# Kernel optimization log

Hardware: AMD Instinct MI355X
Metric: run time of the kernel (lower is better)

## Reference

```python
import jax, jax.numpy as jnp
import numpy as np

N = 50000      # num nodes
HID = 64       # hidden_dim
N2V = 64       # node2vec dim
E = 800000     # num edges
EP = 100000    # prediction edges
L = 2          # num_layers
EPS = 1e-5     # BatchNorm eps


def setup_inputs() -> dict:
    key = jax.random.key(0)
    ks = jax.random.split(key, 8)
    edge_index = jax.random.randint(ks[0], (2, E), 0, N)
    pred_edge = jax.random.randint(ks[1], (EP, 2), 0, N)
    id_emb = jax.random.normal(ks[2], (N, HID), jnp.float32) * 0.1      # learnable ID embedding
    n2v_emb = jax.random.normal(ks[3], (N, N2V), jnp.float32) * 0.1     # frozen node2vec embedding
    proj_w = jax.random.normal(ks[4], (HID + N2V, HID), jnp.float32) / np.sqrt(HID + N2V)
    proj_b = jnp.zeros((HID,), jnp.float32)
    conv_w = jax.random.normal(ks[5], (L, HID, HID), jnp.float32) / np.sqrt(HID)
    conv_b = jnp.zeros((L, HID), jnp.float32)
    bn_gamma = jnp.ones((L, HID), jnp.float32)
    bn_beta = jnp.zeros((L, HID), jnp.float32)
    return {"edge_index": edge_index, "pred_edge": pred_edge, "id_emb": id_emb,
            "n2v_emb": n2v_emb, "proj_w": proj_w, "proj_b": proj_b,
            "conv_w": conv_w, "conv_b": conv_b, "bn_gamma": bn_gamma, "bn_beta": bn_beta}


def reference(edge_index, pred_edge, id_emb, n2v_emb, proj_w, proj_b, conv_w, conv_b, bn_gamma, bn_beta):
    # input projection of concatenated embeddings: [N, HID+N2V] @ [HID+N2V, HID]
    x = jnp.concatenate([id_emb, n2v_emb], axis=1) @ proj_w + proj_b

    # GCN normalization with self-loops: norm_e = d^-1/2[src] * d^-1/2[dst]
    loops = jnp.arange(N, dtype=edge_index.dtype)
    row = jnp.concatenate([edge_index[0], loops])   # source nodes
    col = jnp.concatenate([edge_index[1], loops])   # destination nodes
    deg = jax.ops.segment_sum(jnp.ones(row.shape, x.dtype), col, num_segments=N)
    dis = jnp.where(deg > 0, jax.lax.rsqrt(deg), 0.0)
    norm = dis[row] * dis[col]                      # [E+N]

    for l in range(L):
        h = x @ conv_w[l]                                                    # [N, HID]
        agg = jax.ops.segment_sum(norm[:, None] * h[row], col, num_segments=N) + conv_b[l]
        # BatchNorm1d (training-mode batch stats over nodes)
        mu = agg.mean(axis=0)
        var = agg.var(axis=0)
        xn = (agg - mu) * jax.lax.rsqrt(var + EPS) * bn_gamma[l] + bn_beta[l]
        x = x + jax.nn.relu(xn)                                              # residual (shapes match)

    # dot-product link decoder
    z = x
    return (z[pred_edge[:, 0]] * z[pred_edge[:, 1]]).sum(axis=1)
```

## Files before the change

### kernel.cpp

```cpp
#include <hip/hip_runtime.h>

#define NN 50000
#define HID 64
#define NE 800000
#define NP 100000
#define BN_EPS 1e-5f
#define NB1 196

static inline size_t alignup(size_t x) { return (x + 255) & ~(size_t)255; }

__device__ __forceinline__ void f4fma(float a, const float4& w, float4& c) {
    c.x += a * w.x; c.y += a * w.y; c.z += a * w.z; c.w += a * w.w;
}
__device__ __forceinline__ void f4add(const float4& a, float4& c) {
    c.x += a.x; c.y += a.y; c.z += a.z; c.w += a.w;
}
__device__ __forceinline__ unsigned bfpack(float a, float b) {
    unsigned ua = __float_as_uint(a), ub = __float_as_uint(b);
    ua = (ua + 0x7fffu + ((ua >> 16) & 1u)) >> 16;
    ub = (ub + 0x7fffu + ((ub >> 16) & 1u)) >> 16;
    return ua | (ub << 16);
}
__device__ __forceinline__ float4 bf2f4(uint2 u) {
    float4 r;
    r.x = __uint_as_float(u.x << 16);
    r.y = __uint_as_float(u.x & 0xffff0000u);
    r.z = __uint_as_float(u.y << 16);
    r.w = __uint_as_float(u.y & 0xffff0000u);
    return r;
}


__global__ __launch_bounds__(256) void k_zero(int* __restrict__ cnt, float* __restrict__ sums) {
    int i = blockIdx.x * blockDim.x + threadIdx.x;
    if (i < NN) cnt[i] = 0;
    if (i < 256) sums[i] = 0.f;
}


__global__ __launch_bounds__(256) void k_count(const int* __restrict__ col,
                                               int* __restrict__ cnt, int* __restrict__ rank) {
    int e = blockIdx.x * blockDim.x + threadIdx.x;
    if (e < NE) rank[e] = atomicAdd(&cnt[col[e]], 1);
}


__global__ __launch_bounds__(256) void k_scan1(const int* __restrict__ cnt,
                                               int* __restrict__ offs, int* __restrict__ bsum,
                                               float* __restrict__ dis) {
    __shared__ int s[256];
    int t = threadIdx.x;
    int i = blockIdx.x * 256 + t;
    int v = (i < NN) ? cnt[i] : 0;
    if (i < NN) dis[i] = rsqrtf((float)(v + 1));
    s[t] = v;
    __syncthreads();
    for (int off = 1; off < 256; off <<= 1) {
        int add = (t >= off) ? s[t - off] : 0;
        __syncthreads();
        s[t] += add;
        __syncthreads();
    }
    if (i < NN) offs[i] = s[t] - v;
    if (t == 255) bsum[blockIdx.x] = s[255];
}

__global__ __launch_bounds__(256) void k_scan2(int* __restrict__ bsum, int* __restrict__ boff) {
    __shared__ int s[256];
    int t = threadIdx.x;
    int v = (t < NB1) ? bsum[t] : 0;
    s[t] = v;
    __syncthreads();
    for (int off = 1; off < 256; off <<= 1) {
        int add = (t >= off) ? s[t - off] : 0;
        __syncthreads();
        s[t] += add;
        __syncthreads();
    }
    if (t < NB1) boff[t] = s[t] - v;
}

__global__ __launch_bounds__(256) void k_scan3(int* __restrict__ offs, const int* __restrict__ boff) {
    int i = blockIdx.x * blockDim.x + threadIdx.x;
    if (i < NN) offs[i] += boff[i >> 8];
    if (i == 0) offs[NN] = NE;
}


__global__ __launch_bounds__(256) void k_fill(const int* __restrict__ row, const int* __restrict__ col,
                                              const int* __restrict__ rank, const int* __restrict__ offs,
                                              int* __restrict__ csr_src) {
    int e = blockIdx.x * blockDim.x + threadIdx.x;
    if (e >= NE) return;
    csr_src[offs[col[e]] + rank[e]] = row[e];
}


__global__ __launch_bounds__(256) void k_proj(const float* __restrict__ id_emb,
                                              const float* __restrict__ n2v,
                                              const float* __restrict__ W,
                                              const float* __restrict__ b,
                                              const float* __restrict__ dis,
                                              float* __restrict__ x,
                                              unsigned short* __restrict__ xh) {
    __shared__ float Wl[128 * 64];
    int tid = threadIdx.x;
    for (int i = tid; i < 128 * 64; i += 256) Wl[i] = W[i];
    __syncthreads();
    int sub = tid >> 4, q = tid & 15;
    const float4* W4 = (const float4*)Wl;
    const float4* id4 = (const float4*)id_emb;
    const float4* nv4 = (const float4*)n2v;
    float4* x4 = (float4*)x;
    uint2* xh2 = (uint2*)xh;
    float4 bb = ((const float4*)b)[q];
    const int ngroups = (NN + 63) / 64;
    for (int g = blockIdx.x; g < ngroups; g += gridDim.x) {
        int n0 = g * 64 + sub * 4;
        int r0 = min(n0 + 0, NN - 1), r1 = min(n0 + 1, NN - 1);
        int r2 = min(n0 + 2, NN - 1), r3 = min(n0 + 3, NN - 1);
        float4 c0 = bb, c1 = bb, c2 = bb, c3 = bb;
#pragma unroll 4
        for (int k4 = 0; k4 < 16; ++k4) {
            float4 a0 = id4[r0 * 16 + k4];
            float4 a1 = id4[r1 * 16 + k4];
            float4 a2 = id4[r2 * 16 + k4];
            float4 a3 = id4[r3 * 16 + k4];
            float4 w0 = W4[(k4 * 4 + 0) * 16 + q];
            float4 w1 = W4[(k4 * 4 + 1) * 16 + q];
            float4 w2 = W4[(k4 * 4 + 2) * 16 + q];
            float4 w3 = W4[(k4 * 4 + 3) * 16 + q];
            f4fma(a0.x, w0, c0); f4fma(a0.y, w1, c0); f4fma(a0.z, w2, c0); f4fma(a0.w, w3, c0);
            f4fma(a1.x, w0, c1); f4fma(a1.y, w1, c1); f4fma(a1.z, w2, c1); f4fma(a1.w, w3, c1);
            f4fma(a2.x, w0, c2); f4fma(a2.y, w1, c2); f4fma(a2.z, w2, c2); f4fma(a2.w, w3, c2);
            f4fma(a3.x, w0, c3); f4fma(a3.y, w1, c3); f4fma(a3.z, w2, c3); f4fma(a3.w, w3, c3);
        }
#pragma unroll 4
        for (int k4 = 0; k4 < 16; ++k4) {
            float4 a0 = nv4[r0 * 16 + k4];
            float4 a1 = nv4[r1 * 16 + k4];
            float4 a2 = nv4[r2 * 16 + k4];
            float4 a3 = nv4[r3 * 16 + k4];
            float4 w0 = W4[(k4 * 4 + 64) * 16 + q];
            float4 w1 = W4[(k4 * 4 + 65) * 16 + q];
            float4 w2 = W4[(k4 * 4 + 66) * 16 + q];
            float4 w3 = W4[(k4 * 4 + 67) * 16 + q];
            f4fma(a0.x, w0, c0); f4fma(a0.y, w1, c0); f4fma(a0.z, w2, c0); f4fma(a0.w, w3, c0);
            f4fma(a1.x, w0, c1); f4fma(a1.y, w1, c1); f4fma(a1.z, w2, c1); f4fma(a1.w, w3, c1);
            f4fma(a2.x, w0, c2); f4fma(a2.y, w1, c2); f4fma(a2.z, w2, c2); f4fma(a2.w, w3, c2);
            f4fma(a3.x, w0, c3); f4fma(a3.y, w1, c3); f4fma(a3.z, w2, c3); f4fma(a3.w, w3, c3);
        }
        if (n0 + 0 < NN) { float d = dis[n0+0]; x4[(n0+0)*16+q] = c0;
            xh2[(n0+0)*16+q] = make_uint2(bfpack(c0.x*d,c0.y*d), bfpack(c0.z*d,c0.w*d)); }
        if (n0 + 1 < NN) { float d = dis[n0+1]; x4[(n0+1)*16+q] = c1;
            xh2[(n0+1)*16+q] = make_uint2(bfpack(c1.x*d,c1.y*d), bfpack(c1.z*d,c1.w*d)); }
        if (n0 + 2 < NN) { float d = dis[n0+2]; x4[(n0+2)*16+q] = c2;
            xh2[(n0+2)*16+q] = make_uint2(bfpack(c2.x*d,c2.y*d), bfpack(c2.z*d,c2.w*d)); }
        if (n0 + 3 < NN) { float d = dis[n0+3]; x4[(n0+3)*16+q] = c3;
            xh2[(n0+3)*16+q] = make_uint2(bfpack(c3.x*d,c3.y*d), bfpack(c3.z*d,c3.w*d)); }
    }
}


__global__ __launch_bounds__(256) void k_gather(const int* __restrict__ offs,
                                                const int* __restrict__ csr_src,
                                                const float* __restrict__ dis,
                                                const float* __restrict__ x,
                                                const unsigned short* __restrict__ xh,
                                                unsigned short* __restrict__ th) {
    int gw = (blockIdx.x * blockDim.x + threadIdx.x) >> 6;
    int lane = threadIdx.x & 63;
    int sub = lane >> 4, q = lane & 15;
    int node = gw * 4 + sub;
    if (node >= NN) return;
    const float4* x4 = (const float4*)x;
    const uint2* xh2 = (const uint2*)xh;
    float4 acc = make_float4(0.f, 0.f, 0.f, 0.f);
    int j = offs[node], j1 = offs[node + 1];
    for (; j + 7 < j1; j += 8) {
        int s0 = csr_src[j],     s1 = csr_src[j + 1], s2 = csr_src[j + 2], s3 = csr_src[j + 3];
        int s4 = csr_src[j + 4], s5 = csr_src[j + 5], s6 = csr_src[j + 6], s7 = csr_src[j + 7];
        uint2 u0 = xh2[s0 * 16 + q];
        uint2 u1 = xh2[s1 * 16 + q];
        uint2 u2 = xh2[s2 * 16 + q];
        uint2 u3 = xh2[s3 * 16 + q];
        uint2 u4 = xh2[s4 * 16 + q];
        uint2 u5 = xh2[s5 * 16 + q];
        uint2 u6 = xh2[s6 * 16 + q];
        uint2 u7 = xh2[s7 * 16 + q];
        f4add(bf2f4(u0), acc); f4add(bf2f4(u1), acc);
        f4add(bf2f4(u2), acc); f4add(bf2f4(u3), acc);
        f4add(bf2f4(u4), acc); f4add(bf2f4(u5), acc);
        f4add(bf2f4(u6), acc); f4add(bf2f4(u7), acc);
    }
    for (; j < j1; ++j) {
        uint2 u0 = xh2[csr_src[j] * 16 + q];
        f4add(bf2f4(u0), acc);
    }
    float di = dis[node];
    float4 v = x4[node * 16 + q];
    acc.x = di * (acc.x + di * v.x);
    acc.y = di * (acc.y + di * v.y);
    acc.z = di * (acc.z + di * v.z);
    acc.w = di * (acc.w + di * v.w);
    ((uint2*)th)[node * 16 + q] = make_uint2(bfpack(acc.x, acc.y), bfpack(acc.z, acc.w));
}


__global__ __launch_bounds__(256) void k_gemm_stats(const unsigned short* __restrict__ th,
                                                    const float* __restrict__ W,
                                                    float* __restrict__ agg,
                                                    float* __restrict__ sums) {
    __shared__ float Wl[64 * 64];
    __shared__ float ls0[16][64];
    __shared__ float ls1[16][64];
    int tid = threadIdx.x;
    for (int i = tid; i < 64 * 64; i += 256) Wl[i] = W[i];
    __syncthreads();
    int sub = tid >> 4, q = tid & 15;
    const uint2* t2 = (const uint2*)th;
    const float4* W4 = (const float4*)Wl;
    float4* agg4 = (float4*)agg;
    float4 s1 = make_float4(0.f, 0.f, 0.f, 0.f), s2 = s1;
    const int ngroups = (NN + 63) / 64;
    for (int g = blockIdx.x; g < ngroups; g += gridDim.x) {
        int n0 = g * 64 + sub * 4;
        int r0 = min(n0 + 0, NN - 1), r1 = min(n0 + 1, NN - 1);
        int r2 = min(n0 + 2, NN - 1), r3 = min(n0 + 3, NN - 1);
        float4 c0 = make_float4(0.f,0.f,0.f,0.f), c1 = c0, c2 = c0, c3 = c0;
#pragma unroll 4
        for (int k4 = 0; k4 < 16; ++k4) {
            float4 a0 = bf2f4(t2[r0 * 16 + k4]);
            float4 a1 = bf2f4(t2[r1 * 16 + k4]);
            float4 a2 = bf2f4(t2[r2 * 16 + k4]);
            float4 a3 = bf2f4(t2[r3 * 16 + k4]);
            float4 w0 = W4[(k4 * 4 + 0) * 16 + q];
            float4 w1 = W4[(k4 * 4 + 1) * 16 + q];
            float4 w2 = W4[(k4 * 4 + 2) * 16 + q];
            float4 w3 = W4[(k4 * 4 + 3) * 16 + q];
            f4fma(a0.x, w0, c0); f4fma(a0.y, w1, c0); f4fma(a0.z, w2, c0); f4fma(a0.w, w3, c0);
            f4fma(a1.x, w0, c1); f4fma(a1.y, w1, c1); f4fma(a1.z, w2, c1); f4fma(a1.w, w3, c1);
            f4fma(a2.x, w0, c2); f4fma(a2.y, w1, c2); f4fma(a2.z, w2, c2); f4fma(a2.w, w3, c2);
            f4fma(a3.x, w0, c3); f4fma(a3.y, w1, c3); f4fma(a3.z, w2, c3); f4fma(a3.w, w3, c3);
        }
        if (n0 + 0 < NN) { agg4[(n0 + 0) * 16 + q] = c0;
            s1.x += c0.x; s1.y += c0.y; s1.z += c0.z; s1.w += c0.w;
            s2.x += c0.x*c0.x; s2.y += c0.y*c0.y; s2.z += c0.z*c0.z; s2.w += c0.w*c0.w; }
        if (n0 + 1 < NN) { agg4[(n0 + 1) * 16 + q] = c1;
            s1.x += c1.x; s1.y += c1.y; s1.z += c1.z; s1.w += c1.w;
            s2.x += c1.x*c1.x; s2.y += c1.y*c1.y; s2.z += c1.z*c1.z; s2.w += c1.w*c1.w; }
        if (n0 + 2 < NN) { agg4[(n0 + 2) * 16 + q] = c2;
            s1.x += c2.x; s1.y += c2.y; s1.z += c2.z; s1.w += c2.w;
            s2.x += c2.x*c2.x; s2.y += c2.y*c2.y; s2.z += c2.z*c2.z; s2.w += c2.w*c2.w; }
        if (n0 + 3 < NN) { agg4[(n0 + 3) * 16 + q] = c3;
            s1.x += c3.x; s1.y += c3.y; s1.z += c3.z; s1.w += c3.w;
            s2.x += c3.x*c3.x; s2.y += c3.y*c3.y; s2.z += c3.z*c3.z; s2.w += c3.w*c3.w; }
    }
    ls0[sub][q * 4 + 0] = s1.x; ls0[sub][q * 4 + 1] = s1.y;
    ls0[sub][q * 4 + 2] = s1.z; ls0[sub][q * 4 + 3] = s1.w;
    ls1[sub][q * 4 + 0] = s2.x; ls1[sub][q * 4 + 1] = s2.y;
    ls1[sub][q * 4 + 2] = s2.z; ls1[sub][q * 4 + 3] = s2.w;
    __syncthreads();
    if (tid < 64) {
        float a = 0.f;
#pragma unroll
        for (int r = 0; r < 16; ++r) a += ls0[r][tid];
        atomicAdd(&sums[tid], a);
    } else if (tid < 128) {
        int c = tid - 64;
        float a = 0.f;
#pragma unroll
        for (int r = 0; r < 16; ++r) a += ls1[r][c];
        atomicAdd(&sums[64 + c], a);
    }
}


__global__ __launch_bounds__(256) void k_bnupdate(const float* __restrict__ agg,
                                                  const float* __restrict__ sums,
                                                  const float* __restrict__ gamma,
                                                  const float* __restrict__ beta,
                                                  const float* __restrict__ dis,
                                                  int prescale,
                                                  float* __restrict__ x,
                                                  unsigned short* __restrict__ xh) {
    int i = blockIdx.x * blockDim.x + threadIdx.x;
    if (i >= NN * 16) return;
    int f4 = i & 15;
    const float invn = 1.0f / (float)NN;
    float4 sm = ((const float4*)sums)[f4];
    float4 sq = ((const float4*)(sums + 64))[f4];
    float4 g = ((const float4*)gamma)[f4];
    float4 be = ((const float4*)beta)[f4];
    float4 a = ((const float4*)agg)[i];
    float4 xv = ((const float4*)x)[i];
    float mu, var, rstd, xn;
    mu = sm.x * invn; var = sq.x * invn - mu * mu; rstd = rsqrtf(var + BN_EPS);
    xn = (a.x - mu) * rstd * g.x + be.x; xv.x += fmaxf(xn, 0.f);
    mu = sm.y * invn; var = sq.y * invn - mu * mu; rstd = rsqrtf(var + BN_EPS);
    xn = (a.y - mu) * rstd * g.y + be.y; xv.y += fmaxf(xn, 0.f);
    mu = sm.z * invn; var = sq.z * invn - mu * mu; rstd = rsqrtf(var + BN_EPS);
    xn = (a.z - mu) * rstd * g.z + be.z; xv.z += fmaxf(xn, 0.f);
    mu = sm.w * invn; var = sq.w * invn - mu * mu; rstd = rsqrtf(var + BN_EPS);
    xn = (a.w - mu) * rstd * g.w + be.w; xv.w += fmaxf(xn, 0.f);
    ((float4*)x)[i] = xv;
    float d = prescale ? dis[i >> 4] : 1.0f;
    ((uint2*)xh)[i] = make_uint2(bfpack(xv.x * d, xv.y * d), bfpack(xv.z * d, xv.w * d));
}


__global__ __launch_bounds__(256) void k_decode(const int* __restrict__ pred,
                                                const unsigned short* __restrict__ zh,
                                                float* __restrict__ out) {
    int gw = (blockIdx.x * blockDim.x + threadIdx.x) >> 6;
    int lane = threadIdx.x & 63;
    int sub = lane >> 4, q = lane & 15;
    int p = gw * 4 + sub;
    if (p >= NP) return;
    const uint2* z2 = (const uint2*)zh;
    int a = pred[2 * p], b = pred[2 * p + 1];
    float4 va = bf2f4(z2[a * 16 + q]);
    float4 vb = bf2f4(z2[b * 16 + q]);
    float v = va.x * vb.x + va.y * vb.y + va.z * vb.z + va.w * vb.w;
    v += __shfl_xor(v, 1);
    v += __shfl_xor(v, 2);
    v += __shfl_xor(v, 4);
    v += __shfl_xor(v, 8);
    if (q == 0) out[p] = v;
}

extern "C" void kernel_launch(void* const* d_in, const int* in_sizes, int n_in,
                              void* d_out, int out_size, void* d_ws, size_t ws_size,
                              hipStream_t stream) {
    const int* edge_index = (const int*)d_in[0];
    const int* pred       = (const int*)d_in[1];
    const float* id_emb   = (const float*)d_in[2];
    const float* n2v      = (const float*)d_in[3];
    const float* proj_w   = (const float*)d_in[4];
    const float* proj_b   = (const float*)d_in[5];
    const float* conv_w   = (const float*)d_in[6];
    const float* gamma    = (const float*)d_in[8];
    const float* beta     = (const float*)d_in[9];
    float* out = (float*)d_out;

    char* ws = (char*)d_ws;
    size_t off = 0;
    float* dis   = (float*)(ws + off); off += alignup(NN * 4);
    int* cnt     = (int*)(ws + off);   off += alignup(NN * 4);
    int* offs    = (int*)(ws + off);   off += alignup((NN + 1) * 4);
    int* rank    = (int*)(ws + off);   off += alignup((size_t)NE * 4);
    int* bsum    = (int*)(ws + off);   off += alignup(NB1 * 4);
    int* boff    = (int*)(ws + off);   off += alignup(NB1 * 4);
    int* csr_src = (int*)(ws + off);   off += alignup((size_t)NE * 4);
    float* x     = (float*)(ws + off); off += alignup((size_t)NN * 64 * 4);
    float* agg   = (float*)(ws + off); off += alignup((size_t)NN * 64 * 4);
    unsigned short* xh = (unsigned short*)(ws + off); off += alignup((size_t)NN * 64 * 2);
    unsigned short* th = (unsigned short*)(ws + off); off += alignup((size_t)NN * 64 * 2);
    float* sums  = (float*)(ws + off);

    const int* row = edge_index;
    const int* col = edge_index + NE;

    k_zero<<<NB1, 256, 0, stream>>>(cnt, sums);
    k_count<<<(NE + 255) / 256, 256, 0, stream>>>(col, cnt, rank);
    k_scan1<<<NB1, 256, 0, stream>>>(cnt, offs, bsum, dis);
    k_scan2<<<1, 256, 0, stream>>>(bsum, boff);
    k_scan3<<<NB1, 256, 0, stream>>>(offs, boff);
    k_fill<<<(NE + 255) / 256, 256, 0, stream>>>(row, col, rank, offs, csr_src);

    k_proj<<<512, 256, 0, stream>>>(id_emb, n2v, proj_w, proj_b, dis, x, xh);

    for (int l = 0; l < 2; ++l) {
        k_gather<<<((NN + 3) / 4 * 64 + 255) / 256, 256, 0, stream>>>(offs, csr_src, dis, x, xh, th);
        k_gemm_stats<<<512, 256, 0, stream>>>(th, conv_w + l * 64 * 64, agg, sums + l * 128);
        k_bnupdate<<<(NN * 16 + 255) / 256, 256, 0, stream>>>(agg, sums + l * 128, gamma + l * 64,
                                                              beta + l * 64, dis, (l == 0) ? 1 : 0, x, xh);
    }

    k_decode<<<(NP / 4 * 64 + 255) / 256, 256, 0, stream>>>(pred, xh, out);
}
```

Measured before the change: 207.6 us.

## Fuse neighbor gather into GEMM-stats kernel and replace scan with atomic allocation

The three-kernel prefix scan is replaced by one kernel. Each block scans its own counts locally, then reserves a contiguous CSR range with an atomicAdd on a global cursor. CSR segments are therefore no longer in node order, so the gather reads each node's end from offs plus cnt. The gather and the GEMM/BN-stats kernels are fused so each block aggregates 64 nodes and immediately multiplies them by W. This removes launches and the grid-stride loop, and the self-loop term now reads the bf16 pre-scaled features instead of fp32 x, which slightly changes numerics.

```diff
diff --git a/kernel.cpp b/kernel.cpp
--- a/kernel.cpp
+++ b/kernel.cpp
@@ -31,10 +31,12 @@
 }
 
 
-__global__ __launch_bounds__(256) void k_zero(int* __restrict__ cnt, float* __restrict__ sums) {
+__global__ __launch_bounds__(256) void k_zero(int* __restrict__ cnt, float* __restrict__ sums,
+                                              int* __restrict__ cursor) {
     int i = blockIdx.x * blockDim.x + threadIdx.x;
     if (i < NN) cnt[i] = 0;
     if (i < 256) sums[i] = 0.f;
+    if (i == 0) *cursor = 0;
 }
 
 
@@ -45,10 +47,12 @@
 }
 
 
-__global__ __launch_bounds__(256) void k_scan1(const int* __restrict__ cnt,
-                                               int* __restrict__ offs, int* __restrict__ bsum,
-                                               float* __restrict__ dis) {
+__global__ __launch_bounds__(256) void k_alloc(const int* __restrict__ cnt,
+                                               int* __restrict__ offs,
+                                               float* __restrict__ dis,
+                                               int* __restrict__ cursor) {
     __shared__ int s[256];
+    __shared__ int base;
     int t = threadIdx.x;
     int i = blockIdx.x * 256 + t;
     int v = (i < NN) ? cnt[i] : 0;
@@ -61,29 +65,9 @@
         s[t] += add;
         __syncthreads();
     }
-    if (i < NN) offs[i] = s[t] - v;
-    if (t == 255) bsum[blockIdx.x] = s[255];
-}
-
-__global__ __launch_bounds__(256) void k_scan2(int* __restrict__ bsum, int* __restrict__ boff) {
-    __shared__ int s[256];
-    int t = threadIdx.x;
-    int v = (t < NB1) ? bsum[t] : 0;
-    s[t] = v;
-    __syncthreads();
-    for (int off = 1; off < 256; off <<= 1) {
-        int add = (t >= off) ? s[t - off] : 0;
-        __syncthreads();
-        s[t] += add;
-        __syncthreads();
-    }
-    if (t < NB1) boff[t] = s[t] - v;
-}
-
-__global__ __launch_bounds__(256) void k_scan3(int* __restrict__ offs, const int* __restrict__ boff) {
-    int i = blockIdx.x * blockDim.x + threadIdx.x;
-    if (i < NN) offs[i] += boff[i >> 8];
-    if (i == 0) offs[NN] = NE;
+    if (t == 255) base = atomicAdd(cursor, s[255]);
+    __syncthreads();
+    if (i < NN) offs[i] = base + s[t] - v;
 }
 
 
@@ -162,100 +146,95 @@
 }
 
 
-__global__ __launch_bounds__(256) void k_gather(const int* __restrict__ offs,
-                                                const int* __restrict__ csr_src,
-                                                const float* __restrict__ dis,
-                                                const float* __restrict__ x,
-                                                const unsigned short* __restrict__ xh,
-                                                unsigned short* __restrict__ th) {
-    int gw = (blockIdx.x * blockDim.x + threadIdx.x) >> 6;
-    int lane = threadIdx.x & 63;
-    int sub = lane >> 4, q = lane & 15;
-    int node = gw * 4 + sub;
-    if (node >= NN) return;
-    const float4* x4 = (const float4*)x;
-    const uint2* xh2 = (const uint2*)xh;
-    float4 acc = make_float4(0.f, 0.f, 0.f, 0.f);
-    int j = offs[node], j1 = offs[node + 1];
-    for (; j + 7 < j1; j += 8) {
-        int s0 = csr_src[j],     s1 = csr_src[j + 1], s2 = csr_src[j + 2], s3 = csr_src[j + 3];
-        int s4 = csr_src[j + 4], s5 = csr_src[j + 5], s6 = csr_src[j + 6], s7 = csr_src[j + 7];
-        uint2 u0 = xh2[s0 * 16 + q];
-        uint2 u1 = xh2[s1 * 16 + q];
-        uint2 u2 = xh2[s2 * 16 + q];
-        uint2 u3 = xh2[s3 * 16 + q];
-        uint2 u4 = xh2[s4 * 16 + q];
-        uint2 u5 = xh2[s5 * 16 + q];
-        uint2 u6 = xh2[s6 * 16 + q];
-        uint2 u7 = xh2[s7 * 16 + q];
-        f4add(bf2f4(u0), acc); f4add(bf2f4(u1), acc);
-        f4add(bf2f4(u2), acc); f4add(bf2f4(u3), acc);
-        f4add(bf2f4(u4), acc); f4add(bf2f4(u5), acc);
-        f4add(bf2f4(u6), acc); f4add(bf2f4(u7), acc);
-    }
-    for (; j < j1; ++j) {
-        uint2 u0 = xh2[csr_src[j] * 16 + q];
-        f4add(bf2f4(u0), acc);
-    }
-    float di = dis[node];
-    float4 v = x4[node * 16 + q];
-    acc.x = di * (acc.x + di * v.x);
-    acc.y = di * (acc.y + di * v.y);
-    acc.z = di * (acc.z + di * v.z);
-    acc.w = di * (acc.w + di * v.w);
-    ((uint2*)th)[node * 16 + q] = make_uint2(bfpack(acc.x, acc.y), bfpack(acc.z, acc.w));
-}
-
-
-__global__ __launch_bounds__(256) void k_gemm_stats(const unsigned short* __restrict__ th,
-                                                    const float* __restrict__ W,
-                                                    float* __restrict__ agg,
-                                                    float* __restrict__ sums) {
+__global__ __launch_bounds__(256) void k_gg(const int* __restrict__ offs,
+                                            const int* __restrict__ cnt,
+                                            const int* __restrict__ csr_src,
+                                            const float* __restrict__ dis,
+                                            const unsigned short* __restrict__ xh,
+                                            unsigned short* __restrict__ th,
+                                            const float* __restrict__ W,
+                                            float* __restrict__ agg,
+                                            float* __restrict__ sums) {
     __shared__ float Wl[64 * 64];
     __shared__ float ls0[16][64];
     __shared__ float ls1[16][64];
     int tid = threadIdx.x;
     for (int i = tid; i < 64 * 64; i += 256) Wl[i] = W[i];
+    int node0 = blockIdx.x * 64;
+    const uint2* xh2 = (const uint2*)xh;
+    uint2* th2 = (uint2*)th;
+    {
+        int wave = tid >> 6, lane = tid & 63;
+        int gsub = lane >> 4, q = lane & 15;
+        for (int r = 0; r < 4; ++r) {
+            int node = node0 + wave * 16 + r * 4 + gsub;
+            if (node < NN) {
+                float4 acc = make_float4(0.f, 0.f, 0.f, 0.f);
+                int j = offs[node], j1 = j + cnt[node];
+                for (; j + 7 < j1; j += 8) {
+                    int s0 = csr_src[j],     s1 = csr_src[j + 1], s2 = csr_src[j + 2], s3 = csr_src[j + 3];
+                    int s4 = csr_src[j + 4], s5 = csr_src[j + 5], s6 = csr_src[j + 6], s7 = csr_src[j + 7];
+                    uint2 u0 = xh2[s0 * 16 + q];
+                    uint2 u1 = xh2[s1 * 16 + q];
+                    uint2 u2 = xh2[s2 * 16 + q];
+                    uint2 u3 = xh2[s3 * 16 + q];
+                    uint2 u4 = xh2[s4 * 16 + q];
+                    uint2 u5 = xh2[s5 * 16 + q];
+                    uint2 u6 = xh2[s6 * 16 + q];
+                    uint2 u7 = xh2[s7 * 16 + q];
+                    f4add(bf2f4(u0), acc); f4add(bf2f4(u1), acc);
+                    f4add(bf2f4(u2), acc); f4add(bf2f4(u3), acc);
+                    f4add(bf2f4(u4), acc); f4add(bf2f4(u5), acc);
+                    f4add(bf2f4(u6), acc); f4add(bf2f4(u7), acc);
+                }
+                for (; j < j1; ++j) {
+                    uint2 u0 = xh2[csr_src[j] * 16 + q];
+                    f4add(bf2f4(u0), acc);
+                }
+                f4add(bf2f4(xh2[node * 16 + q]), acc);
+                float di = dis[node];
+                acc.x *= di; acc.y *= di; acc.z *= di; acc.w *= di;
+                th2[node * 16 + q] = make_uint2(bfpack(acc.x, acc.y), bfpack(acc.z, acc.w));
+            }
+        }
+    }
     __syncthreads();
     int sub = tid >> 4, q = tid & 15;
     const uint2* t2 = (const uint2*)th;
     const float4* W4 = (const float4*)Wl;
     float4* agg4 = (float4*)agg;
-    float4 s1 = make_float4(0.f, 0.f, 0.f, 0.f), s2 = s1;
-    const int ngroups = (NN + 63) / 64;
-    for (int g = blockIdx.x; g < ngroups; g += gridDim.x) {
-        int n0 = g * 64 + sub * 4;
-        int r0 = min(n0 + 0, NN - 1), r1 = min(n0 + 1, NN - 1);
-        int r2 = min(n0 + 2, NN - 1), r3 = min(n0 + 3, NN - 1);
-        float4 c0 = make_float4(0.f,0.f,0.f,0.f), c1 = c0, c2 = c0, c3 = c0;
+    int n0 = node0 + sub * 4;
+    int r0 = min(n0 + 0, NN - 1), r1 = min(n0 + 1, NN - 1);
+    int r2 = min(n0 + 2, NN - 1), r3 = min(n0 + 3, NN - 1);
+    float4 c0 = make_float4(0.f,0.f,0.f,0.f), c1 = c0, c2 = c0, c3 = c0;
 #pragma unroll 4
-        for (int k4 = 0; k4 < 16; ++k4) {
-            float4 a0 = bf2f4(t2[r0 * 16 + k4]);
-            float4 a1 = bf2f4(t2[r1 * 16 + k4]);
-            float4 a2 = bf2f4(t2[r2 * 16 + k4]);
-            float4 a3 = bf2f4(t2[r3 * 16 + k4]);
-            float4 w0 = W4[(k4 * 4 + 0) * 16 + q];
-            float4 w1 = W4[(k4 * 4 + 1) * 16 + q];
-            float4 w2 = W4[(k4 * 4 + 2) * 16 + q];
-            float4 w3 = W4[(k4 * 4 + 3) * 16 + q];
-            f4fma(a0.x, w0, c0); f4fma(a0.y, w1, c0); f4fma(a0.z, w2, c0); f4fma(a0.w, w3, c0);
-            f4fma(a1.x, w0, c1); f4fma(a1.y, w1, c1); f4fma(a1.z, w2, c1); f4fma(a1.w, w3, c1);
-            f4fma(a2.x, w0, c2); f4fma(a2.y, w1, c2); f4fma(a2.z, w2, c2); f4fma(a2.w, w3, c2);
-            f4fma(a3.x, w0, c3); f4fma(a3.y, w1, c3); f4fma(a3.z, w2, c3); f4fma(a3.w, w3, c3);
-        }
-        if (n0 + 0 < NN) { agg4[(n0 + 0) * 16 + q] = c0;
-            s1.x += c0.x; s1.y += c0.y; s1.z += c0.z; s1.w += c0.w;
-            s2.x += c0.x*c0.x; s2.y += c0.y*c0.y; s2.z += c0.z*c0.z; s2.w += c0.w*c0.w; }
-        if (n0 + 1 < NN) { agg4[(n0 + 1) * 16 + q] = c1;
-            s1.x += c1.x; s1.y += c1.y; s1.z += c1.z; s1.w += c1.w;
-            s2.x += c1.x*c1.x; s2.y += c1.y*c1.y; s2.z += c1.z*c1.z; s2.w += c1.w*c1.w; }
-        if (n0 + 2 < NN) { agg4[(n0 + 2) * 16 + q] = c2;
-            s1.x += c2.x; s1.y += c2.y; s1.z += c2.z; s1.w += c2.w;
-            s2.x += c2.x*c2.x; s2.y += c2.y*c2.y; s2.z += c2.z*c2.z; s2.w += c2.w*c2.w; }
-        if (n0 + 3 < NN) { agg4[(n0 + 3) * 16 + q] = c3;
-            s1.x += c3.x; s1.y += c3.y; s1.z += c3.z; s1.w += c3.w;
-            s2.x += c3.x*c3.x; s2.y += c3.y*c3.y; s2.z += c3.z*c3.z; s2.w += c3.w*c3.w; }
-    }
+    for (int k4 = 0; k4 < 16; ++k4) {
+        float4 a0 = bf2f4(t2[r0 * 16 + k4]);
+        float4 a1 = bf2f4(t2[r1 * 16 + k4]);
+        float4 a2 = bf2f4(t2[r2 * 16 + k4]);
+        float4 a3 = bf2f4(t2[r3 * 16 + k4]);
+        float4 w0 = W4[(k4 * 4 + 0) * 16 + q];
+        float4 w1 = W4[(k4 * 4 + 1) * 16 + q];
+        float4 w2 = W4[(k4 * 4 + 2) * 16 + q];
+        float4 w3 = W4[(k4 * 4 + 3) * 16 + q];
+        f4fma(a0.x, w0, c0); f4fma(a0.y, w1, c0); f4fma(a0.z, w2, c0); f4fma(a0.w, w3, c0);
+        f4fma(a1.x, w0, c1); f4fma(a1.y, w1, c1); f4fma(a1.z, w2, c1); f4fma(a1.w, w3, c1);
+        f4fma(a2.x, w0, c2); f4fma(a2.y, w1, c2); f4fma(a2.z, w2, c2); f4fma(a2.w, w3, c2);
+        f4fma(a3.x, w0, c3); f4fma(a3.y, w1, c3); f4fma(a3.z, w2, c3); f4fma(a3.w, w3, c3);
+    }
+    float4 s1 = make_float4(0.f,0.f,0.f,0.f), s2 = s1;
+    if (n0 + 0 < NN) { agg4[(n0 + 0) * 16 + q] = c0;
+        s1.x += c0.x; s1.y += c0.y; s1.z += c0.z; s1.w += c0.w;
+        s2.x += c0.x*c0.x; s2.y += c0.y*c0.y; s2.z += c0.z*c0.z; s2.w += c0.w*c0.w; }
+    if (n0 + 1 < NN) { agg4[(n0 + 1) * 16 + q] = c1;
+        s1.x += c1.x; s1.y += c1.y; s1.z += c1.z; s1.w += c1.w;
+        s2.x += c1.x*c1.x; s2.y += c1.y*c1.y; s2.z += c1.z*c1.z; s2.w += c1.w*c1.w; }
+    if (n0 + 2 < NN) { agg4[(n0 + 2) * 16 + q] = c2;
+        s1.x += c2.x; s1.y += c2.y; s1.z += c2.z; s1.w += c2.w;
+        s2.x += c2.x*c2.x; s2.y += c2.y*c2.y; s2.z += c2.z*c2.z; s2.w += c2.w*c2.w; }
+    if (n0 + 3 < NN) { agg4[(n0 + 3) * 16 + q] = c3;
+        s1.x += c3.x; s1.y += c3.y; s1.z += c3.z; s1.w += c3.w;
+        s2.x += c3.x*c3.x; s2.y += c3.y*c3.y; s2.z += c3.z*c3.z; s2.w += c3.w*c3.w; }
     ls0[sub][q * 4 + 0] = s1.x; ls0[sub][q * 4 + 1] = s1.y;
     ls0[sub][q * 4 + 2] = s1.z; ls0[sub][q * 4 + 3] = s1.w;
     ls1[sub][q * 4 + 0] = s2.x; ls1[sub][q * 4 + 1] = s2.y;
@@ -347,10 +326,9 @@
     size_t off = 0;
     float* dis   = (float*)(ws + off); off += alignup(NN * 4);
     int* cnt     = (int*)(ws + off);   off += alignup(NN * 4);
-    int* offs    = (int*)(ws + off);   off += alignup((NN + 1) * 4);
+    int* offs    = (int*)(ws + off);   off += alignup(NN * 4);
     int* rank    = (int*)(ws + off);   off += alignup((size_t)NE * 4);
-    int* bsum    = (int*)(ws + off);   off += alignup(NB1 * 4);
-    int* boff    = (int*)(ws + off);   off += alignup(NB1 * 4);
+    int* cursor  = (int*)(ws + off);   off += alignup(4);
     int* csr_src = (int*)(ws + off);   off += alignup((size_t)NE * 4);
     float* x     = (float*)(ws + off); off += alignup((size_t)NN * 64 * 4);
     float* agg   = (float*)(ws + off); off += alignup((size_t)NN * 64 * 4);
@@ -361,18 +339,16 @@
     const int* row = edge_index;
     const int* col = edge_index + NE;
 
-    k_zero<<<NB1, 256, 0, stream>>>(cnt, sums);
+    k_zero<<<NB1, 256, 0, stream>>>(cnt, sums, cursor);
     k_count<<<(NE + 255) / 256, 256, 0, stream>>>(col, cnt, rank);
-    k_scan1<<<NB1, 256, 0, stream>>>(cnt, offs, bsum, dis);
-    k_scan2<<<1, 256, 0, stream>>>(bsum, boff);
-    k_scan3<<<NB1, 256, 0, stream>>>(offs, boff);
+    k_alloc<<<NB1, 256, 0, stream>>>(cnt, offs, dis, cursor);
     k_fill<<<(NE + 255) / 256, 256, 0, stream>>>(row, col, rank, offs, csr_src);
 
     k_proj<<<512, 256, 0, stream>>>(id_emb, n2v, proj_w, proj_b, dis, x, xh);
 
     for (int l = 0; l < 2; ++l) {
-        k_gather<<<((NN + 3) / 4 * 64 + 255) / 256, 256, 0, stream>>>(offs, csr_src, dis, x, xh, th);
-        k_gemm_stats<<<512, 256, 0, stream>>>(th, conv_w + l * 64 * 64, agg, sums + l * 128);
+        k_gg<<<(NN + 63) / 64, 256, 0, stream>>>(offs, cnt, csr_src, dis, xh, th,
+                                                 conv_w + l * 64 * 64, agg, sums + l * 128);
         k_bnupdate<<<(NN * 16 + 255) / 256, 256, 0, stream>>>(agg, sums + l * 128, gamma + l * 64,
                                                               beta + l * 64, dis, (l == 0) ? 1 : 0, x, xh);
     }
```

New measurement: 218.3 us. 5.2% more time.
